# Performance work log

Hardware: AMD Instinct MI355X
Metric: run time of the kernel (lower is better)

The kernel has to match this reference:

```python
import jax, jax.numpy as jnp
import numpy as np


def _igd(x, pf):
    # pf: [M, d] reference front, x: [N, d] candidate set
    # squared Euclidean distances via ||a||^2 + ||b||^2 - 2 a.b (cdist expansion)
    pf_sq = jnp.sum(pf * pf, axis=1, keepdims=True)          # [M, 1]
    x_sq = jnp.sum(x * x, axis=1, keepdims=True).T            # [1, N]
    cross = pf @ x.T                                          # [M, N]
    d2 = jnp.maximum(pf_sq + x_sq - 2.0 * cross, 0.0)
    dist = jnp.sqrt(d2)                                       # [M, N]
    # IGD: mean over reference points of min distance to candidate set
    return jnp.mean(jnp.min(dist, axis=1))


def setup_inputs() -> dict:
    key = jax.random.key(0)
    k1, k2 = jax.random.split(key)
    N, M, D = 16384, 16384, 64
    x = jax.random.normal(k1, (N, D), dtype=jnp.float32)
    pf = jax.random.normal(k2, (M, D), dtype=jnp.float32)
    return {"x": x, "pf": pf}


def reference(x, pf):
    return _igd(x, pf)
```

## Files before the change

kernel.cpp:

```cpp
#include <hip/hip_runtime.h>


typedef float f32x16 __attribute__((ext_vector_type(16)));
typedef float f32x2 __attribute__((ext_vector_type(2)));
typedef int i32x8 __attribute__((ext_vector_type(8)));
typedef unsigned long long u64;

#define DIM 64
#define NSPLIT 12
#define UNITB 2048
#define CHUNKU 8
#define CHUNKB (CHUNKU * UNITB)
#define MTILE 256

union BFrag { u64 q[4]; i32x8 v; };

__device__ __forceinline__ void g2lds16(const void* g, void* l) {
    __builtin_amdgcn_global_load_lds(
        (const __attribute__((address_space(1))) unsigned int*)g,
        (__attribute__((address_space(3))) unsigned int*)l, 16, 0, 0);
}
__device__ __forceinline__ void g2lds4(const void* g, void* l) {
    __builtin_amdgcn_global_load_lds(
        (const __attribute__((address_space(1))) unsigned int*)g,
        (__attribute__((address_space(3))) unsigned int*)l, 4, 0, 0);
}

__device__ __forceinline__ float vmin3(float a, float b, float c) {
    float d;
    asm("v_min3_f32 %0, %1, %2, %3" : "=v"(d) : "v"(a), "v"(b), "v"(c));
    return d;
}

__device__ __forceinline__ void encode16(const float* f, u64 w[2], float& sumsq) {
    unsigned int w32[4];
#pragma unroll
    for (int k = 0; k < 4; ++k) {
        int lo = __builtin_amdgcn_cvt_pk_fp8_f32(f[4 * k],     f[4 * k + 1], 0,  false);
        w32[k] = __builtin_amdgcn_cvt_pk_fp8_f32(f[4 * k + 2], f[4 * k + 3], lo, true);
    }
#pragma unroll
    for (int k = 0; k < 4; ++k) {
        f32x2 d0 = __builtin_amdgcn_cvt_pk_f32_fp8(w32[k], false);
        f32x2 d1 = __builtin_amdgcn_cvt_pk_f32_fp8(w32[k], true);
        sumsq += d0.x * d0.x + d0.y * d0.y + d1.x * d1.x + d1.y * d1.y;
    }
    w[0] = (u64)w32[0] | ((u64)w32[1] << 32);
    w[1] = (u64)w32[2] | ((u64)w32[3] << 32);
}

__global__ void pack_kernel(const float* __restrict__ x, const float* __restrict__ pf,
                            unsigned char* __restrict__ Bp, unsigned char* __restrict__ Ab,
                            float* __restrict__ xsq, float* __restrict__ pfsq,
                            float* __restrict__ out, int N, int M) {
    int gid = blockIdx.x * blockDim.x + threadIdx.x;
    if (gid == 0) out[0] = 0.f;
    if (gid < N * 4) {
        int col = gid >> 2, t = gid & 3;
        const float* s = x + (size_t)col * DIM + t * 16;
        float4 v0 = *(const float4*)(s);
        float4 v1 = *(const float4*)(s + 4);
        float4 v2 = *(const float4*)(s + 8);
        float4 v3 = *(const float4*)(s + 12);
        float f[16] = {v0.x, v0.y, v0.z, v0.w, v1.x, v1.y, v1.z, v1.w,
                       v2.x, v2.y, v2.z, v2.w, v3.x, v3.y, v3.z, v3.w};
        float partial = 0.f;
        u64 w[2];
        encode16(f, w, partial);
        int u = col >> 5, c31 = col & 31;
        unsigned char* ub = Bp + (size_t)u * UNITB;
        int h = t >> 1;
#pragma unroll
        for (int ss = 0; ss < 2; ++ss) {
            int q = (t & 1) * 2 + ss;
            *(u64*)(ub + (size_t)q * 512 + (size_t)(h * 32 + c31) * 8) = w[ss];
        }
        partial += __shfl_xor(partial, 1);
        partial += __shfl_xor(partial, 2);
        if (t == 0) xsq[col] = partial;
    } else {
        int g = gid - N * 4;
        int row = g >> 2, q = g & 3;
        if (row >= M) return;
        const float* s = pf + (size_t)row * DIM + q * 16;
        float4 v0 = *(const float4*)(s);
        float4 v1 = *(const float4*)(s + 4);
        float4 v2 = *(const float4*)(s + 8);
        float4 v3 = *(const float4*)(s + 12);
        float f[16] = {v0.x, v0.y, v0.z, v0.w, v1.x, v1.y, v1.z, v1.w,
                       v2.x, v2.y, v2.z, v2.w, v3.x, v3.y, v3.z, v3.w};
#pragma unroll
        for (int j = 0; j < 16; ++j) f[j] *= -2.f;
        float partial = 0.f;
        u64 w[2];
        encode16(f, w, partial);
        *(u64*)(Ab + (size_t)row * DIM + q * 16)     = w[0];
        *(u64*)(Ab + (size_t)row * DIM + q * 16 + 8) = w[1];
        partial += __shfl_xor(partial, 1);
        partial += __shfl_xor(partial, 2);
        if (q == 0) pfsq[row] = partial * 0.25f;
    }
}

__global__ __launch_bounds__(256, 3)
void igd_main(const unsigned char* __restrict__ A, const unsigned char* __restrict__ Bp,
              const float* __restrict__ xsq, float* __restrict__ partial, int N) {
    __shared__ unsigned char ldsB[2][CHUNKB];
    __shared__ float ldsX[2][CHUNKU * 32];
    const int tid = threadIdx.x;
    const int mTile  = blockIdx.x;
    const int nsplit = blockIdx.y;
    const int lane = tid & 63;
    const int wave = tid >> 6;
    const int half = lane >> 5;
    const int l31  = lane & 31;
    const int rowBase = mTile * MTILE + wave * 64;

    const int utotal = N / 32;
    const int ubase  = utotal / NSPLIT;
    const int urem   = utotal % NSPLIT;
    const int ustart = nsplit * ubase + (nsplit < urem ? nsplit : urem);
    const int ucount = ubase + (nsplit < urem ? 1 : 0);
    const int nch = (ucount + CHUNKU - 1) / CHUNKU;

    BFrag a[2];
#pragma unroll
    for (int g = 0; g < 2; ++g) {
        const unsigned char* ap = A + (size_t)(rowBase + 32 * g + l31) * DIM + half * 32;
#pragma unroll
        for (int qq = 0; qq < 4; ++qq)
            a[g].q[qq] = *(const u64*)(ap + qq * 8);
    }

    const unsigned char* gB = Bp + (size_t)ustart * UNITB;
    const float* gX = xsq + ustart * 32;

#define STAGE(c, buf)                                                          \
    {                                                                          \
        int bytes = (ucount - (c) * CHUNKU) < CHUNKU ? (ucount - (c) * CHUNKU) * UNITB : CHUNKB; \
        const unsigned char* src = gB + (size_t)(c) * CHUNKB;                  \
        _Pragma("unroll")                                                      \
        for (int i = 0; i < 4; ++i) {                                          \
            int off = i * 4096 + tid * 16;                                     \
            if (off < bytes)                                                   \
                g2lds16(src + off, &ldsB[buf][off]);                           \
        }                                                                      \
        int xcnt = bytes >> 6;                                                 \
        if (tid < xcnt)                                                        \
            g2lds4(gX + (c) * (CHUNKU * 32) + tid, &ldsX[buf][tid]);           \
    }

    f32x16 zero, m0, m1;
#pragma unroll
    for (int r = 0; r < 16; ++r) { zero[r] = 0.f; m0[r] = 1e30f; m1[r] = 1e30f; }

#define LOADF(rr, lb, u)                                                       \
    {                                                                          \
        const unsigned char* p = (lb) + (u) * UNITB;                           \
        rr.q[0] = *(const u64*)(p);                                            \
        rr.q[1] = *(const u64*)(p + 512);                                      \
        rr.q[2] = *(const u64*)(p + 1024);                                     \
        rr.q[3] = *(const u64*)(p + 1536);                                     \
    }

#define MFMA2(accA, accB, bfrag)                                               \
    {                                                                          \
        accA = __builtin_amdgcn_mfma_scale_f32_32x32x64_f8f6f4(                \
            a[0].v, bfrag.v, zero, 0, 0, 0, 0x7F7F7F7F, 0, 0x7F7F7F7F);        \
        accB = __builtin_amdgcn_mfma_scale_f32_32x32x64_f8f6f4(                \
            a[1].v, bfrag.v, zero, 0, 0, 0, 0x7F7F7F7F, 0, 0x7F7F7F7F);        \
    }

#define MINS3(pA0, pA1, pB0, pB1, xa, xb)                                      \
    {                                                                          \
        f32x2 va; va[0] = (xa); va[1] = (xa);                                  \
        f32x2 vb; vb[0] = (xb); vb[1] = (xb);                                  \
        _Pragma("unroll")                                                      \
        for (int r = 0; r < 8; ++r) {                                          \
            f32x2 tA0 = { pA0[2 * r], pA0[2 * r + 1] }; tA0 = tA0 + va;        \
            f32x2 tB0 = { pB0[2 * r], pB0[2 * r + 1] }; tB0 = tB0 + vb;        \
            m0[2 * r]     = vmin3(m0[2 * r],     tA0[0], tB0[0]);              \
            m0[2 * r + 1] = vmin3(m0[2 * r + 1], tA0[1], tB0[1]);              \
            f32x2 tA1 = { pA1[2 * r], pA1[2 * r + 1] }; tA1 = tA1 + va;        \
            f32x2 tB1 = { pB1[2 * r], pB1[2 * r + 1] }; tB1 = tB1 + vb;        \
            m1[2 * r]     = vmin3(m1[2 * r],     tA1[0], tB1[0]);              \
            m1[2 * r + 1] = vmin3(m1[2 * r + 1], tA1[1], tB1[1]);              \
        }                                                                      \
    }

#define MINS(accA, accB, xq)                                                   \
    {                                                                          \
        _Pragma("unroll")                                                      \
        for (int r = 0; r < 16; ++r) {                                         \
            m0[r] = fminf(m0[r], accA[r] + (xq));                              \
            m1[r] = fminf(m1[r], accB[r] + (xq));                              \
        }                                                                      \
    }

    STAGE(0, 0);
    __syncthreads();

    for (int c = 0; c < nch; ++c) {
        const int buf = c & 1;
        if (c + 1 < nch) STAGE(c + 1, buf ^ 1);
        const int cnt = (ucount - c * CHUNKU) < CHUNKU ? (ucount - c * CHUNKU) : CHUNKU;
        const unsigned char* lb = &ldsB[buf][0] + lane * 8;
        const float* lx = &ldsX[buf][0] + l31;
        if (cnt == CHUNKU) {
            BFrag b0, b1;
#pragma unroll
            for (int u = 0; u < CHUNKU; u += 2) {
                LOADF(b0, lb, u);
                LOADF(b1, lb, u + 1);
                f32x16 acA0, acA1, acB0, acB1;
                MFMA2(acA0, acA1, b0);
                MFMA2(acB0, acB1, b1);
                const float xa = lx[u * 32];
                const float xb = lx[(u + 1) * 32];
                MINS3(acA0, acA1, acB0, acB1, xa, xb);
            }
        } else {
            BFrag bt;
            for (int u = 0; u < cnt; ++u) {
                LOADF(bt, lb, u);
                f32x16 t0, t1;
                MFMA2(t0, t1, bt);
                MINS(t0, t1, lx[u * 32]);
            }
        }
        __syncthreads();
    }
#undef STAGE
#undef LOADF
#undef MFMA2
#undef MINS3
#undef MINS

#pragma unroll
    for (int mask = 1; mask <= 16; mask <<= 1) {
#pragma unroll
        for (int r = 0; r < 16; ++r) {
            m0[r] = fminf(m0[r], __shfl_xor(m0[r], mask));
            m1[r] = fminf(m1[r], __shfl_xor(m1[r], mask));
        }
    }
    if (l31 == 0) {
#pragma unroll
        for (int r = 0; r < 16; ++r) {
            int row0 = rowBase + (r & 3) + 8 * (r >> 2) + 4 * half;
            partial[(size_t)row0 * NSPLIT + nsplit] = m0[r];
            partial[(size_t)(row0 + 32) * NSPLIT + nsplit] = m1[r];
        }
    }
}

__global__ void reduce_kernel(const float* __restrict__ partial, const float* __restrict__ pfsq,
                              float* __restrict__ out, int M, float invM) {
    int row = blockIdx.x * blockDim.x + threadIdx.x;
    float v = 0.f;
    if (row < M) {
        const float* p = partial + (size_t)row * NSPLIT;
        float mn = 3.4e38f;
#pragma unroll
        for (int s = 0; s < NSPLIT; ++s) mn = fminf(mn, p[s]);
        float d2 = mn + pfsq[row];
        v = sqrtf(fmaxf(d2, 0.f)) * invM;
    }
#pragma unroll
    for (int m = 1; m < 64; m <<= 1) v += __shfl_xor(v, m);
    __shared__ float wsum[4];
    int lane = threadIdx.x & 63, w = threadIdx.x >> 6;
    if (lane == 0) wsum[w] = v;
    __syncthreads();
    if (threadIdx.x == 0) atomicAdd(out, wsum[0] + wsum[1] + wsum[2] + wsum[3]);
}

extern "C" void kernel_launch(void* const* d_in, const int* in_sizes, int n_in,
                              void* d_out, int out_size, void* d_ws, size_t ws_size,
                              hipStream_t stream) {
    const float* x  = (const float*)d_in[0];
    const float* pf = (const float*)d_in[1];
    const int N = in_sizes[0] / DIM;
    const int M = in_sizes[1] / DIM;

    char* ws = (char*)d_ws;
    unsigned char* Bp = (unsigned char*)ws;
    unsigned char* Ab = (unsigned char*)(ws + (size_t)N * DIM);
    float* xsq  = (float*)(ws + (size_t)(N + M) * DIM);
    float* pfsq = xsq + N;
    float* part = pfsq + M;

    int packThreads = (N + M) * 4;
    pack_kernel<<<dim3((packThreads + 255) / 256), 256, 0, stream>>>(
        x, pf, Bp, Ab, xsq, pfsq, (float*)d_out, N, M);
    igd_main<<<dim3(M / MTILE, NSPLIT), 256, 0, stream>>>(Ab, Bp, xsq, part, N);
    reduce_kernel<<<dim3((M + 255) / 256), 256, 0, stream>>>(part, pfsq, (float*)d_out, M, 1.f / (float)M);
}
```

Baseline: 89.03 us.

## Replace LDS double-buffered staging with direct global loads and register prefetch

Drops the shared-memory double buffer and the block-wide barriers. Each wave now loads its B fragments and x-norm values straight from global memory into registers, prefetching four units ahead. The aim is to remove LDS traffic and `__syncthreads` stalls in the distance/min loop. In exchange, every wave in a block fetches the same B data separately, which relies on L2/L1 hits. The paired v_min3 reduction is also replaced by plain fminf. The prefetch reads up to four units past each split's range, which for the last split goes past the end of the input buffers.

```diff
diff --git a/kernel.cpp b/kernel.cpp
--- a/kernel.cpp
+++ b/kernel.cpp
@@ -9,28 +9,9 @@
 #define DIM 64
 #define NSPLIT 12
 #define UNITB 2048
-#define CHUNKU 8
-#define CHUNKB (CHUNKU * UNITB)
 #define MTILE 256
 
 union BFrag { u64 q[4]; i32x8 v; };
-
-__device__ __forceinline__ void g2lds16(const void* g, void* l) {
-    __builtin_amdgcn_global_load_lds(
-        (const __attribute__((address_space(1))) unsigned int*)g,
-        (__attribute__((address_space(3))) unsigned int*)l, 16, 0, 0);
-}
-__device__ __forceinline__ void g2lds4(const void* g, void* l) {
-    __builtin_amdgcn_global_load_lds(
-        (const __attribute__((address_space(1))) unsigned int*)g,
-        (__attribute__((address_space(3))) unsigned int*)l, 4, 0, 0);
-}
-
-__device__ __forceinline__ float vmin3(float a, float b, float c) {
-    float d;
-    asm("v_min3_f32 %0, %1, %2, %3" : "=v"(d) : "v"(a), "v"(b), "v"(c));
-    return d;
-}
 
 __device__ __forceinline__ void encode16(const float* f, u64 w[2], float& sumsq) {
     unsigned int w32[4];
@@ -105,8 +86,6 @@
 __global__ __launch_bounds__(256, 3)
 void igd_main(const unsigned char* __restrict__ A, const unsigned char* __restrict__ Bp,
               const float* __restrict__ xsq, float* __restrict__ partial, int N) {
-    __shared__ unsigned char ldsB[2][CHUNKB];
-    __shared__ float ldsX[2][CHUNKU * 32];
     const int tid = threadIdx.x;
     const int mTile  = blockIdx.x;
     const int nsplit = blockIdx.y;
@@ -121,7 +100,6 @@
     const int urem   = utotal % NSPLIT;
     const int ustart = nsplit * ubase + (nsplit < urem ? nsplit : urem);
     const int ucount = ubase + (nsplit < urem ? 1 : 0);
-    const int nch = (ucount + CHUNKU - 1) / CHUNKU;
 
     BFrag a[2];
 #pragma unroll
@@ -132,36 +110,21 @@
             a[g].q[qq] = *(const u64*)(ap + qq * 8);
     }
 
-    const unsigned char* gB = Bp + (size_t)ustart * UNITB;
-    const float* gX = xsq + ustart * 32;
-
-#define STAGE(c, buf)                                                          \
+    const unsigned char* bG = Bp + (size_t)ustart * UNITB + lane * 8;
+    const float* xG = xsq + ustart * 32 + l31;
+
+#define LOADG(rr, u)                                                           \
     {                                                                          \
-        int bytes = (ucount - (c) * CHUNKU) < CHUNKU ? (ucount - (c) * CHUNKU) * UNITB : CHUNKB; \
-        const unsigned char* src = gB + (size_t)(c) * CHUNKB;                  \
-        _Pragma("unroll")                                                      \
-        for (int i = 0; i < 4; ++i) {                                          \
-            int off = i * 4096 + tid * 16;                                     \
-            if (off < bytes)                                                   \
-                g2lds16(src + off, &ldsB[buf][off]);                           \
-        }                                                                      \
-        int xcnt = bytes >> 6;                                                 \
-        if (tid < xcnt)                                                        \
-            g2lds4(gX + (c) * (CHUNKU * 32) + tid, &ldsX[buf][tid]);           \
-    }
-
-    f32x16 zero, m0, m1;
-#pragma unroll
-    for (int r = 0; r < 16; ++r) { zero[r] = 0.f; m0[r] = 1e30f; m1[r] = 1e30f; }
-
-#define LOADF(rr, lb, u)                                                       \
-    {                                                                          \
-        const unsigned char* p = (lb) + (u) * UNITB;                           \
+        const unsigned char* p = bG + (size_t)(u) * UNITB;                     \
         rr.q[0] = *(const u64*)(p);                                            \
         rr.q[1] = *(const u64*)(p + 512);                                      \
         rr.q[2] = *(const u64*)(p + 1024);                                     \
         rr.q[3] = *(const u64*)(p + 1536);                                     \
     }
+
+    f32x16 zero, m0, m1;
+#pragma unroll
+    for (int r = 0; r < 16; ++r) { zero[r] = 0.f; m0[r] = 1e30f; m1[r] = 1e30f; }
 
 #define MFMA2(accA, accB, bfrag)                                               \
     {                                                                          \
@@ -171,69 +134,45 @@
             a[1].v, bfrag.v, zero, 0, 0, 0, 0x7F7F7F7F, 0, 0x7F7F7F7F);        \
     }
 
-#define MINS3(pA0, pA1, pB0, pB1, xa, xb)                                      \
-    {                                                                          \
-        f32x2 va; va[0] = (xa); va[1] = (xa);                                  \
-        f32x2 vb; vb[0] = (xb); vb[1] = (xb);                                  \
-        _Pragma("unroll")                                                      \
-        for (int r = 0; r < 8; ++r) {                                          \
-            f32x2 tA0 = { pA0[2 * r], pA0[2 * r + 1] }; tA0 = tA0 + va;        \
-            f32x2 tB0 = { pB0[2 * r], pB0[2 * r + 1] }; tB0 = tB0 + vb;        \
-            m0[2 * r]     = vmin3(m0[2 * r],     tA0[0], tB0[0]);              \
-            m0[2 * r + 1] = vmin3(m0[2 * r + 1], tA0[1], tB0[1]);              \
-            f32x2 tA1 = { pA1[2 * r], pA1[2 * r + 1] }; tA1 = tA1 + va;        \
-            f32x2 tB1 = { pB1[2 * r], pB1[2 * r + 1] }; tB1 = tB1 + vb;        \
-            m1[2 * r]     = vmin3(m1[2 * r],     tA1[0], tB1[0]);              \
-            m1[2 * r + 1] = vmin3(m1[2 * r + 1], tA1[1], tB1[1]);              \
-        }                                                                      \
-    }
-
-#define MINS(accA, accB, xq)                                                   \
+#define MINS(accA, accB, xq0)                                                  \
     {                                                                          \
         _Pragma("unroll")                                                      \
         for (int r = 0; r < 16; ++r) {                                         \
-            m0[r] = fminf(m0[r], accA[r] + (xq));                              \
-            m1[r] = fminf(m1[r], accB[r] + (xq));                              \
+            m0[r] = fminf(m0[r], accA[r] + (xq0));                             \
+            m1[r] = fminf(m1[r], accB[r] + (xq0));                             \
         }                                                                      \
     }
 
-    STAGE(0, 0);
-    __syncthreads();
-
-    for (int c = 0; c < nch; ++c) {
-        const int buf = c & 1;
-        if (c + 1 < nch) STAGE(c + 1, buf ^ 1);
-        const int cnt = (ucount - c * CHUNKU) < CHUNKU ? (ucount - c * CHUNKU) : CHUNKU;
-        const unsigned char* lb = &ldsB[buf][0] + lane * 8;
-        const float* lx = &ldsX[buf][0] + l31;
-        if (cnt == CHUNKU) {
-            BFrag b0, b1;
-#pragma unroll
-            for (int u = 0; u < CHUNKU; u += 2) {
-                LOADF(b0, lb, u);
-                LOADF(b1, lb, u + 1);
-                f32x16 acA0, acA1, acB0, acB1;
-                MFMA2(acA0, acA1, b0);
-                MFMA2(acB0, acB1, b1);
-                const float xa = lx[u * 32];
-                const float xb = lx[(u + 1) * 32];
-                MINS3(acA0, acA1, acB0, acB1, xa, xb);
-            }
-        } else {
-            BFrag bt;
-            for (int u = 0; u < cnt; ++u) {
-                LOADF(bt, lb, u);
-                f32x16 t0, t1;
-                MFMA2(t0, t1, bt);
-                MINS(t0, t1, lx[u * 32]);
-            }
-        }
-        __syncthreads();
-    }
-#undef STAGE
-#undef LOADF
+    BFrag b[4];
+    float xq[4];
+#pragma unroll
+    for (int i = 0; i < 4; ++i) {
+        LOADG(b[i], i);
+        xq[i] = xG[(size_t)i * 32];
+    }
+
+    const int umain = ucount & ~3;
+    for (int u = 0; u < umain; u += 4) {
+#pragma unroll
+        for (int s = 0; s < 4; ++s) {
+            f32x16 acA, acB;
+            MFMA2(acA, acB, b[s]);
+            const float x0 = xq[s];
+            LOADG(b[s], u + 4 + s);
+            xq[s] = xG[(size_t)(u + 4 + s) * 32];
+            MINS(acA, acB, x0);
+        }
+    }
+#pragma unroll
+    for (int s = 0; s < 3; ++s) {
+        if (umain + s < ucount) {
+            f32x16 acA, acB;
+            MFMA2(acA, acB, b[s]);
+            MINS(acA, acB, xq[s]);
+        }
+    }
+#undef LOADG
 #undef MFMA2
-#undef MINS3
 #undef MINS
 
 #pragma unroll
```

Measured after the change: 87.29 us. No clear change (-2.0%).
